# Kernel tuning notes

Measured on AMD Instinct MI355X. Metric: run time of the kernel, lower is better.

Reference implementation:

```python
import jax, jax.numpy as jnp
import numpy as np
from jax import lax

T, B, D = 64, 1024, 1024

def setup_inputs() -> dict:
    key = jax.random.key(0)
    k1, k2, k3, k4 = jax.random.split(key, 4)
    pred_states = jax.random.normal(k1, (T, B, D), dtype=jnp.float32)
    true_states = jax.random.normal(k2, (T, B, D), dtype=jnp.float32)
    # nn.Linear(D, D): weight [D, D], bias [D]
    lim = 1.0 / np.sqrt(D)
    W = jax.random.uniform(k3, (D, D), dtype=jnp.float32, minval=-lim, maxval=lim)
    b = jax.random.uniform(k4, (D,), dtype=jnp.float32, minval=-lim, maxval=lim)
    return {"pred_states": pred_states, "true_states": true_states, "W": W, "b": b}

def reference(pred_states, true_states, W, b):
    # carry: (accumulated loss [B,D], gating weight [B,D])
    def step(carry, xs):
        loss, weight = carry
        pred, true = xs
        se = (pred - true) ** 2                      # elementwise MSE, reduction='none'
        loss = loss + weight * se
        logits = se @ W.T + b                        # Linear(attention_size, attention_size)
        weight = se * jax.nn.softmax(logits, axis=-1)  # AttentionNet gating
        return (loss, weight), None

    init = (jnp.zeros_like(pred_states[0]), jnp.ones_like(pred_states[0]))
    (loss, _), _ = lax.scan(step, init, (pred_states, true_states))
    return loss
```

## Files before the change

kernel.cpp:

```cpp
#include <hip/hip_runtime.h>
#include <hip/hip_fp16.h>

typedef _Float16 f16x4 __attribute__((ext_vector_type(4)));
typedef _Float16 f16x8 __attribute__((ext_vector_type(8)));
typedef float    f32x4 __attribute__((ext_vector_type(4)));

#define TBD 67108864ull
#define BD  1048576ull

#define ASM_VMCNT(N) asm volatile("s_waitcnt vmcnt(" #N ")" ::: "memory")
#define ASM_LGKM(N)  asm volatile("s_waitcnt lgkmcnt(" #N ")" ::: "memory")
#define BARRIER()    __builtin_amdgcn_s_barrier()
#define MFMA(a,b,c)  __builtin_amdgcn_mfma_f32_16x16x32_f16((a),(b),(c),0,0,0)

__global__ __launch_bounds__(256) void se_split_k(const float* __restrict__ pred,
                                                  const float* __restrict__ tru,
                                                  const float* __restrict__ W,
                                                  _Float16* __restrict__ hi,
                                                  _Float16* __restrict__ W_hi) {
  if (blockIdx.x < 1024) {
    size_t wi = ((size_t)blockIdx.x * 256 + threadIdx.x) * 4;
    float4 x = *(const float4*)(W + wi);
    f16x4 h;
    h[0] = (_Float16)x.x; h[1] = (_Float16)x.y; h[2] = (_Float16)x.z; h[3] = (_Float16)x.w;
    *(f16x4*)(W_hi + wi) = h;
  }
  size_t stride = (size_t)gridDim.x * 1024;
  for (size_t i = ((size_t)blockIdx.x * 256 + threadIdx.x) * 4; i < TBD; i += stride) {
    float4 p = *(const float4*)(pred + i);
    float4 t = *(const float4*)(tru + i);
    f16x4 h;
    h[0] = (_Float16)((p.x - t.x) * (p.x - t.x));
    h[1] = (_Float16)((p.y - t.y) * (p.y - t.y));
    h[2] = (_Float16)((p.z - t.z) * (p.z - t.z));
    h[3] = (_Float16)((p.w - t.w) * (p.w - t.w));
    *(f16x4*)(hi + i) = h;
  }
}


#define GL2_A(dstb, kof)                                                          \
  _Pragma("unroll")                                                               \
  for (int q = 0; q < 2; ++q)                                                     \
    __builtin_amdgcn_global_load_lds(                                             \
        (const __attribute__((address_space(1))) void*)(aSrc[q] + (kof)),         \
        (__attribute__((address_space(3))) void*)((dstb) + q * 4096 + tid * 16),  \
        16, 0, 0);

#define GL4_B(dstb, kof)                                                          \
  _Pragma("unroll")                                                               \
  for (int q = 0; q < 4; ++q)                                                     \
    __builtin_amdgcn_global_load_lds(                                             \
        (const __attribute__((address_space(1))) void*)(bSrc[q] + (kof)),         \
        (__attribute__((address_space(3))) void*)((dstb) + 8192 + q * 4096 + tid * 16), \
        16, 0, 0);

#define MCL(j0, B0, B1)                                  \
  __builtin_amdgcn_s_setprio(1);                         \
  acc[0][(j0)]   = MFMA(a0, B0, acc[0][(j0)]);           \
  acc[1][(j0)]   = MFMA(a1, B0, acc[1][(j0)]);           \
  acc[2][(j0)]   = MFMA(a2, B0, acc[2][(j0)]);           \
  acc[3][(j0)]   = MFMA(a3, B0, acc[3][(j0)]);           \
  acc[0][(j0)+1] = MFMA(a0, B1, acc[0][(j0)+1]);         \
  acc[1][(j0)+1] = MFMA(a1, B1, acc[1][(j0)+1]);         \
  acc[2][(j0)+1] = MFMA(a2, B1, acc[2][(j0)+1]);         \
  acc[3][(j0)+1] = MFMA(a3, B1, acc[3][(j0)+1]);         \
  __builtin_amdgcn_s_setprio(0);

#define LD(buf, off) (*(const f16x8*)((buf) + (off)))

__global__ __launch_bounds__(256, 2) void gemm_logits_k(
    const _Float16* __restrict__ Ah, const _Float16* __restrict__ Wh,
    const float* __restrict__ bias, float* __restrict__ C) {
  __shared__ uint4 lds4[3072];
  char* lds = (char*)lds4;
  const int tid = threadIdx.x;
  const int lane = tid & 63;
  const int wid = tid >> 6;
  const int wm = wid >> 1;
  const int wn = wid & 1;

  const int bid = blockIdx.x;
  const int wgid = (bid & 7) * 256 + (bid >> 3);
  const int bm = wgid >> 2, bn = wgid & 3;
  const int row0 = bm * 128, col0 = bn * 256;

  const _Float16* aSrc[2];
  const _Float16* bSrc[4];
#pragma unroll
  for (int q = 0; q < 2; ++q) {
    int p = q * 4096 + tid * 16;
    int srow = p >> 7;
    int s = (p >> 4) & 7;
    int sig = s ^ (srow & 7);
    int row = 2 * srow + (sig >> 2);
    aSrc[q] = Ah + ((size_t)(row0 + row) * 1024 + (size_t)(sig & 3) * 8);
  }
#pragma unroll
  for (int q = 0; q < 4; ++q) {
    int p = q * 4096 + tid * 16;
    int srow = p >> 7;
    int s = (p >> 4) & 7;
    int sig = s ^ (srow & 7);
    int row = 2 * srow + (sig >> 2);
    bSrc[q] = Wh + ((size_t)(col0 + row) * 1024 + (size_t)(sig & 3) * 8);
  }

  const int u = lane >> 4;
  const int hr = (lane & 15) >> 1;
  const int ls = u + 4 * (lane & 1);
  const int aoff = (wm * 32 + hr) * 128 + ((ls ^ hr) * 16);
  const int boff = 8192 + (wn * 64 + hr) * 128 + ((ls ^ hr) * 16);

  f32x4 acc[4][8] = {};

  char* buf0 = lds;
  char* buf1 = lds + 24576;
  GL2_A(buf0, 0)
  GL4_B(buf0, 0)
  GL2_A(buf1, 32)
  GL4_B(buf1, 32)
  ASM_VMCNT(6);
  BARRIER();

#pragma unroll 1
  for (int t = 0; t < 32; ++t) {
    char* ldsb = lds + (t & 1) * 24576;
    const int tt = (t + 2 < 32) ? t + 2 : 31;
    const size_t kof = (size_t)tt * 32;

    f16x8 a0 = LD(ldsb, aoff + 0 * 1024);
    f16x8 a1 = LD(ldsb, aoff + 1 * 1024);
    f16x8 a2 = LD(ldsb, aoff + 2 * 1024);
    f16x8 a3 = LD(ldsb, aoff + 3 * 1024);
    f16x8 b0 = LD(ldsb, boff + 0 * 1024);
    f16x8 b1 = LD(ldsb, boff + 1 * 1024);
    f16x8 b2 = LD(ldsb, boff + 2 * 1024);
    f16x8 b3 = LD(ldsb, boff + 3 * 1024);
    f16x8 b4 = LD(ldsb, boff + 4 * 1024);
    f16x8 b5 = LD(ldsb, boff + 5 * 1024);
    f16x8 b6 = LD(ldsb, boff + 6 * 1024);
    f16x8 b7 = LD(ldsb, boff + 7 * 1024);
    ASM_LGKM(6);
    MCL(0, b0, b1)
    ASM_LGKM(4);
    MCL(2, b2, b3)
    ASM_LGKM(2);
    MCL(4, b4, b5)
    ASM_LGKM(0);
    BARRIER();
    GL2_A(ldsb, kof)
    GL4_B(ldsb, kof)
    MCL(6, b6, b7)
    ASM_VMCNT(6);
    BARRIER();
  }
  ASM_VMCNT(0);

#pragma unroll
  for (int fj = 0; fj < 8; ++fj) {
    int c = col0 + wn * 128 + fj * 16 + (lane & 15);
    float bj = bias[c];
#pragma unroll
    for (int fi = 0; fi < 4; ++fi) {
      int r = row0 + wm * 64 + fi * 16 + u * 4;
#pragma unroll
      for (int q = 0; q < 4; ++q)
        C[(size_t)(r + q) * 1024 + c] = acc[fi][fj][q] + bj;
    }
  }
}

__global__ __launch_bounds__(256) void softmax_loss_k(const float* __restrict__ logits,
                                                      const _Float16* __restrict__ hi,
                                                      float* __restrict__ out) {
  const int b = blockIdx.x;
  const int tid = threadIdx.x, lane = tid & 63, wid = tid >> 6;
  __shared__ float red[8];
  float4 wprev = make_float4(1.f, 1.f, 1.f, 1.f);
  float4 lacc  = make_float4(0.f, 0.f, 0.f, 0.f);

  size_t base = (size_t)b * 1024;
  float4 x = ((const float4*)(logits + base))[tid];
  f16x4  h = ((const f16x4*)(hi + base))[tid];

#pragma unroll 1
  for (int t = 0; t < 64; ++t) {
    float4 se;
    se.x = (float)h[0];
    se.y = (float)h[1];
    se.z = (float)h[2];
    se.w = (float)h[3];
    lacc.x += wprev.x * se.x;
    lacc.y += wprev.y * se.y;
    lacc.z += wprev.z * se.z;
    lacc.w += wprev.w * se.w;

    int tn = (t + 1 < 64) ? t + 1 : t;
    size_t nbase = ((size_t)tn * 1024 + (size_t)b) * 1024;
    float4 xn = ((const float4*)(logits + nbase))[tid];
    f16x4  hn = ((const f16x4*)(hi + nbase))[tid];

    float m = fmaxf(fmaxf(x.x, x.y), fmaxf(x.z, x.w));
#pragma unroll
    for (int o = 32; o >= 1; o >>= 1) m = fmaxf(m, __shfl_xor(m, o, 64));
    if (lane == 0) red[wid] = m;
    __syncthreads();
    m = fmaxf(fmaxf(red[0], red[1]), fmaxf(red[2], red[3]));
    float e0 = __expf(x.x - m), e1 = __expf(x.y - m), e2 = __expf(x.z - m), e3 = __expf(x.w - m);
    float s = (e0 + e1) + (e2 + e3);
#pragma unroll
    for (int o = 32; o >= 1; o >>= 1) s += __shfl_xor(s, o, 64);
    if (lane == 0) red[4 + wid] = s;
    __syncthreads();
    s = (red[4] + red[5]) + (red[6] + red[7]);
    float inv = 1.0f / s;

    wprev.x = se.x * e0 * inv;
    wprev.y = se.y * e1 * inv;
    wprev.z = se.z * e2 * inv;
    wprev.w = se.w * e3 * inv;

    x = xn; h = hn;
  }
  ((float4*)(out + (size_t)b * 1024))[tid] = lacc;
}

extern "C" void kernel_launch(void* const* d_in, const int* in_sizes, int n_in,
                              void* d_out, int out_size, void* d_ws, size_t ws_size,
                              hipStream_t stream) {
  const float* pred = (const float*)d_in[0];
  const float* tru  = (const float*)d_in[1];
  const float* W    = (const float*)d_in[2];
  const float* bias = (const float*)d_in[3];
  float* out = (float*)d_out;

  char* ws = (char*)d_ws;
  _Float16* se_hi  = (_Float16*)(ws);
  float*    logits = (float*)   (ws + 134217728ull);
  _Float16* W_hi   = (_Float16*)(ws + 402653184ull);

  se_split_k<<<2048, 256, 0, stream>>>(pred, tru, W, se_hi, W_hi);
  gemm_logits_k<<<2048, 256, 0, stream>>>(se_hi, W_hi, bias, logits);
  softmax_loss_k<<<1024, 256, 0, stream>>>(logits, se_hi, out);
}
```

Measured before the change: 379.0 us.

## Store logits as fp16 pairs in a permuted layout and widen se conversion loads

The GEMM epilogue now writes logits as packed fp16 pairs (columns c and c+64) instead of fp32. This halves the 256MB logits write and the matching read in the softmax kernel, and the softmax kernel's column mapping is changed to match the packed layout. The se conversion kernel also processes 8 elements per thread with 16-byte fp16 stores. The cost is fp16 rounding of the logits before softmax, plus scattered 4-byte stores and 2-element se loads in place of the earlier wider vector accesses.

```diff
diff --git a/kernel.cpp b/kernel.cpp
--- a/kernel.cpp
+++ b/kernel.cpp
@@ -1,6 +1,7 @@
 #include <hip/hip_runtime.h>
 #include <hip/hip_fp16.h>
 
+typedef _Float16 f16x2 __attribute__((ext_vector_type(2)));
 typedef _Float16 f16x4 __attribute__((ext_vector_type(4)));
 typedef _Float16 f16x8 __attribute__((ext_vector_type(8)));
 typedef float    f32x4 __attribute__((ext_vector_type(4)));
@@ -25,16 +26,22 @@
     h[0] = (_Float16)x.x; h[1] = (_Float16)x.y; h[2] = (_Float16)x.z; h[3] = (_Float16)x.w;
     *(f16x4*)(W_hi + wi) = h;
   }
-  size_t stride = (size_t)gridDim.x * 1024;
-  for (size_t i = ((size_t)blockIdx.x * 256 + threadIdx.x) * 4; i < TBD; i += stride) {
-    float4 p = *(const float4*)(pred + i);
-    float4 t = *(const float4*)(tru + i);
-    f16x4 h;
-    h[0] = (_Float16)((p.x - t.x) * (p.x - t.x));
-    h[1] = (_Float16)((p.y - t.y) * (p.y - t.y));
-    h[2] = (_Float16)((p.z - t.z) * (p.z - t.z));
-    h[3] = (_Float16)((p.w - t.w) * (p.w - t.w));
-    *(f16x4*)(hi + i) = h;
+  size_t stride = (size_t)gridDim.x * 2048;
+  for (size_t i = ((size_t)blockIdx.x * 256 + threadIdx.x) * 8; i < TBD; i += stride) {
+    float4 p0 = *(const float4*)(pred + i);
+    float4 p1 = *(const float4*)(pred + i + 4);
+    float4 t0 = *(const float4*)(tru + i);
+    float4 t1 = *(const float4*)(tru + i + 4);
+    f16x8 h;
+    h[0] = (_Float16)((p0.x - t0.x) * (p0.x - t0.x));
+    h[1] = (_Float16)((p0.y - t0.y) * (p0.y - t0.y));
+    h[2] = (_Float16)((p0.z - t0.z) * (p0.z - t0.z));
+    h[3] = (_Float16)((p0.w - t0.w) * (p0.w - t0.w));
+    h[4] = (_Float16)((p1.x - t1.x) * (p1.x - t1.x));
+    h[5] = (_Float16)((p1.y - t1.y) * (p1.y - t1.y));
+    h[6] = (_Float16)((p1.z - t1.z) * (p1.z - t1.z));
+    h[7] = (_Float16)((p1.w - t1.w) * (p1.w - t1.w));
+    *(f16x8*)(hi + i) = h;
   }
 }
 
@@ -71,7 +78,7 @@
 
 __global__ __launch_bounds__(256, 2) void gemm_logits_k(
     const _Float16* __restrict__ Ah, const _Float16* __restrict__ Wh,
-    const float* __restrict__ bias, float* __restrict__ C) {
+    const float* __restrict__ bias, unsigned int* __restrict__ C16) {
   __shared__ uint4 lds4[3072];
   char* lds = (char*)lds4;
   const int tid = threadIdx.x;
@@ -157,57 +164,71 @@
   }
   ASM_VMCNT(0);
 
-#pragma unroll
-  for (int fj = 0; fj < 8; ++fj) {
-    int c = col0 + wn * 128 + fj * 16 + (lane & 15);
-    float bj = bias[c];
+  const int span = (col0 + wn * 128) >> 7;
+#pragma unroll
+  for (int fj = 0; fj < 4; ++fj) {
+    int x = fj * 16 + (lane & 15);
+    int cl = col0 + wn * 128 + x;
+    float bjl = bias[cl];
+    float bjh = bias[cl + 64];
 #pragma unroll
     for (int fi = 0; fi < 4; ++fi) {
       int r = row0 + wm * 64 + fi * 16 + u * 4;
 #pragma unroll
-      for (int q = 0; q < 4; ++q)
-        C[(size_t)(r + q) * 1024 + c] = acc[fi][fj][q] + bj;
+      for (int q = 0; q < 4; ++q) {
+        f16x2 v;
+        v[0] = (_Float16)(acc[fi][fj][q] + bjl);
+        v[1] = (_Float16)(acc[fi][fj + 4][q] + bjh);
+        C16[(size_t)(r + q) * 512 + span * 64 + x] = __builtin_bit_cast(unsigned int, v);
+      }
     }
   }
 }
 
-__global__ __launch_bounds__(256) void softmax_loss_k(const float* __restrict__ logits,
+__global__ __launch_bounds__(256) void softmax_loss_k(const unsigned int* __restrict__ L16,
                                                       const _Float16* __restrict__ hi,
                                                       float* __restrict__ out) {
   const int b = blockIdx.x;
   const int tid = threadIdx.x, lane = tid & 63, wid = tid >> 6;
   __shared__ float red[8];
+  const int cA = (tid >> 5) * 128 + ((2 * tid) & 63);
+  const int cB = cA + 64;
+
   float4 wprev = make_float4(1.f, 1.f, 1.f, 1.f);
   float4 lacc  = make_float4(0.f, 0.f, 0.f, 0.f);
 
   size_t base = (size_t)b * 1024;
-  float4 x = ((const float4*)(logits + base))[tid];
-  f16x4  h = ((const f16x4*)(hi + base))[tid];
+  uint2 lg  = *(const uint2*)(L16 + (size_t)b * 512 + 2 * tid);
+  f16x2 sA  = *(const f16x2*)(hi + base + cA);
+  f16x2 sB  = *(const f16x2*)(hi + base + cB);
 
 #pragma unroll 1
   for (int t = 0; t < 64; ++t) {
     float4 se;
-    se.x = (float)h[0];
-    se.y = (float)h[1];
-    se.z = (float)h[2];
-    se.w = (float)h[3];
+    f16x2 p0 = __builtin_bit_cast(f16x2, lg.x);
+    f16x2 p1 = __builtin_bit_cast(f16x2, lg.y);
+    se.x = (float)sA[0]; se.y = (float)sA[1];
+    se.z = (float)sB[0]; se.w = (float)sB[1];
     lacc.x += wprev.x * se.x;
     lacc.y += wprev.y * se.y;
     lacc.z += wprev.z * se.z;
     lacc.w += wprev.w * se.w;
 
     int tn = (t + 1 < 64) ? t + 1 : t;
-    size_t nbase = ((size_t)tn * 1024 + (size_t)b) * 1024;
-    float4 xn = ((const float4*)(logits + nbase))[tid];
-    f16x4  hn = ((const f16x4*)(hi + nbase))[tid];
-
-    float m = fmaxf(fmaxf(x.x, x.y), fmaxf(x.z, x.w));
+    size_t nrow = (size_t)tn * 1024 + (size_t)b;
+    uint2 lgn = *(const uint2*)(L16 + nrow * 512 + 2 * tid);
+    f16x2 sAn = *(const f16x2*)(hi + nrow * 1024 + cA);
+    f16x2 sBn = *(const f16x2*)(hi + nrow * 1024 + cB);
+
+    float xA0 = (float)p0[0], xB0 = (float)p0[1];
+    float xA1 = (float)p1[0], xB1 = (float)p1[1];
+    float m = fmaxf(fmaxf(xA0, xA1), fmaxf(xB0, xB1));
 #pragma unroll
     for (int o = 32; o >= 1; o >>= 1) m = fmaxf(m, __shfl_xor(m, o, 64));
     if (lane == 0) red[wid] = m;
     __syncthreads();
     m = fmaxf(fmaxf(red[0], red[1]), fmaxf(red[2], red[3]));
-    float e0 = __expf(x.x - m), e1 = __expf(x.y - m), e2 = __expf(x.z - m), e3 = __expf(x.w - m);
+    float e0 = __expf(xA0 - m), e1 = __expf(xA1 - m), e2 = __expf(xB0 - m), e3 = __expf(xB1 - m);
     float s = (e0 + e1) + (e2 + e3);
 #pragma unroll
     for (int o = 32; o >= 1; o >>= 1) s += __shfl_xor(s, o, 64);
@@ -221,9 +242,12 @@
     wprev.z = se.z * e2 * inv;
     wprev.w = se.w * e3 * inv;
 
-    x = xn; h = hn;
-  }
-  ((float4*)(out + (size_t)b * 1024))[tid] = lacc;
+    lg = lgn; sA = sAn; sB = sBn;
+  }
+  float2 oA = make_float2(lacc.x, lacc.y);
+  float2 oB = make_float2(lacc.z, lacc.w);
+  *(float2*)(out + (size_t)b * 1024 + cA) = oA;
+  *(float2*)(out + (size_t)b * 1024 + cB) = oB;
 }
 
 extern "C" void kernel_launch(void* const* d_in, const int* in_sizes, int n_in,
@@ -236,11 +260,11 @@
   float* out = (float*)d_out;
 
   char* ws = (char*)d_ws;
-  _Float16* se_hi  = (_Float16*)(ws);
-  float*    logits = (float*)   (ws + 134217728ull);
-  _Float16* W_hi   = (_Float16*)(ws + 402653184ull);
+  _Float16*     se_hi = (_Float16*)(ws);
+  unsigned int* L16   = (unsigned int*)(ws + 134217728ull);
+  _Float16*     W_hi  = (_Float16*)(ws + 268435456ull);
 
   se_split_k<<<2048, 256, 0, stream>>>(pred, tru, W, se_hi, W_hi);
-  gemm_logits_k<<<2048, 256, 0, stream>>>(se_hi, W_hi, bias, logits);
-  softmax_loss_k<<<1024, 256, 0, stream>>>(logits, se_hi, out);
-}
+  gemm_logits_k<<<2048, 256, 0, stream>>>(se_hi, W_hi, bias, L16);
+  softmax_loss_k<<<1024, 256, 0, stream>>>(L16, se_hi, out);
+}
```

New measurement: 334.9 us. 11.7% less time.
